# Optimization experiments

Hardware: AMD Instinct MI355X
Metric: run time of the kernel (lower is better)

## Reference

```python
import jax, jax.numpy as jnp
import numpy as np

B, T, D, V = 2, 2048, 768, 50257
REWARD_SCALE = 0.5
DIV_WEIGHT = 0.1
EPS = 1e-8  # torch cosine_similarity eps


def setup_inputs() -> dict:
    key = jax.random.key(0)
    k1, k2, k3, k4 = jax.random.split(key, 4)
    return {
        "pass2_hidden": jax.random.normal(k1, (B, T, D), dtype=jnp.float32),
        "pass3_hidden": jax.random.normal(k2, (B, T, D), dtype=jnp.float32),
        "W": jax.random.normal(k3, (V, D), dtype=jnp.float32) * 0.02,  # lm_head weight [V, D]
        "targets": jax.random.randint(k4, (B, T), 0, V, dtype=jnp.int64),
    }


def _masked_ce(hidden, W, targets):
    # hidden: [B,T,D], W: [V,D], targets: [B,T] with ignore_index=-1
    logits = jnp.einsum('btd,vd->btv', hidden, W).reshape(B * T, V)
    t = targets.reshape(B * T)
    valid = t != -1
    safe_t = jnp.where(valid, t, 0)
    logp = jax.nn.log_softmax(logits, axis=-1)
    nll = -jnp.take_along_axis(logp, safe_t[:, None], axis=-1)[:, 0]
    nll = jnp.where(valid, nll, 0.0)
    return nll.sum() / jnp.maximum(valid.sum(), 1).astype(nll.dtype)


def reference(pass2_hidden, pass3_hidden, W, targets):
    # pass 2 CE computed under no_grad in the original
    loss_p2 = jax.lax.stop_gradient(_masked_ce(pass2_hidden, W, targets))
    loss_p3 = _masked_ce(pass3_hidden, W, targets)
    reward_loss = -REWARD_SCALE * (loss_p2 - loss_p3)

    p2 = jax.lax.stop_gradient(pass2_hidden.reshape(B * T, D))  # .detach()
    p3 = pass3_hidden.reshape(B * T, D)
    n2 = jnp.maximum(jnp.linalg.norm(p2, axis=-1), EPS)
    n3 = jnp.maximum(jnp.linalg.norm(p3, axis=-1), EPS)
    cos = jnp.sum(p2 * p3, axis=-1) / (n2 * n3)
    divergence_loss = DIV_WEIGHT * cos.mean()
    return reward_loss + divergence_loss
```

## Files before the change

kernel.cpp:

```cpp
#include <hip/hip_runtime.h>
#include <math.h>

#define BT     4096
#define M_TOT  8192
#define KDIM   768
#define VDIM   50257
#define NBLK   393
#define KCH    24
#define REWARD_SCALE 0.5
#define DIV_WEIGHT   0.1
#define EPS_COS      1e-8f
#define LOG2E        1.44269504088896340736f

typedef _Float16 half8 __attribute__((ext_vector_type(8)));
typedef float    f32x4 __attribute__((ext_vector_type(4)));

#define A_FRAGS (64*KCH*8*64)
#define W_FRAGS (NBLK*KCH*8*64)

__device__ __forceinline__ void g2l16(const short* g, short* l) {
    __builtin_amdgcn_global_load_lds(
        (const __attribute__((address_space(1))) unsigned int*)(const void*)g,
        (__attribute__((address_space(3))) unsigned int*)(void*)l,
        16, 0, 0);
}

__global__ __launch_bounds__(256)
void convert_A_kernel(const float* __restrict__ p2, const float* __restrict__ p3,
                      short* __restrict__ Ahi)
{
    __shared__ float Ls[128][36];
    const int mb = blockIdx.x;
    const int k0 = blockIdx.y;
    const int tid = threadIdx.x;

#pragma unroll
    for (int p = 0; p < 4; ++p) {
        int i = p * 1024 + tid * 4;
        int r = i >> 5;
        int c = i & 31;
        int m = mb * 128 + r;
        const float* src = (m < BT) ? (p2 + (size_t)m * KDIM)
                                    : (p3 + (size_t)(m - BT) * KDIM);
        float4 v = *(const float4*)(src + k0 * 32 + c);
        *(float4*)&Ls[r][c] = v;
    }
    __syncthreads();

    size_t base = ((size_t)(mb * KCH + k0) * 8) * 64;
#pragma unroll
    for (int h = 0; h < 2; ++h) {
        int f    = tid + h * 256;
        int lane = f & 63;
        int tile = f >> 6;
        int row  = tile * 16 + (lane & 15);
        int kq   = (lane >> 4) * 8;
        half8 out;
#pragma unroll
        for (int j = 0; j < 8; ++j) out[j] = (_Float16)Ls[row][kq + j];
        *(half8*)(Ahi + (base + f) * 8) = out;
    }
}

__global__ __launch_bounds__(256)
void convert_W_kernel(const float* __restrict__ W, short* __restrict__ Whi)
{
    __shared__ float Ls[128][36];
    const int nb = blockIdx.x;
    const int k0 = blockIdx.y;
    const int tid = threadIdx.x;

#pragma unroll
    for (int p = 0; p < 4; ++p) {
        int i = p * 1024 + tid * 4;
        int r = i >> 5;
        int c = i & 31;
        int v = nb * 128 + r;
        float4 val = make_float4(0.f, 0.f, 0.f, 0.f);
        if (v < VDIM) val = *(const float4*)(W + (size_t)v * KDIM + k0 * 32 + c);
        *(float4*)&Ls[r][c] = val;
    }
    __syncthreads();

    size_t base = ((size_t)(nb * KCH + k0) * 8) * 64;
#pragma unroll
    for (int h = 0; h < 2; ++h) {
        int f    = tid + h * 256;
        int lane = f & 63;
        int tile = f >> 6;
        int row  = tile * 16 + (lane & 15);
        int kq   = (lane >> 4) * 8;
        half8 out;
#pragma unroll
        for (int j = 0; j < 8; ++j) out[j] = (_Float16)(Ls[row][kq + j] * LOG2E);
        *(half8*)(Whi + (base + f) * 8) = out;
    }
}

__global__ __launch_bounds__(256, 4)
void gemm_f16_kernel(const short* __restrict__ Ahi, const short* __restrict__ Whi,
                     double* __restrict__ g_sumexp)
{
    __shared__ __align__(16) short As[2][8][64][8];
    __shared__ float rowsum[128];

    const int tid    = threadIdx.x;
    const int lane   = tid & 63;
    const int wave   = tid >> 6;
    const int wave_m = wave >> 1;
    const int wave_n = wave & 1;
    const int mb = blockIdx.x;
    const int nb = blockIdx.y;

    if (tid < 128) rowsum[tid] = 0.0f;

    f32x4 acc[4][4];
#pragma unroll
    for (int i = 0; i < 4; ++i)
#pragma unroll
        for (int j = 0; j < 4; ++j) acc[i][j] = (f32x4)0.0f;

    const short* Ablk  = Ahi + (size_t)mb * KCH * 4096 + lane * 8;
    const short* Bbase = Whi + (size_t)nb * KCH * 4096
                             + ((size_t)(wave_n * 4) * 64 + lane) * 8;

#define STAGEA(k0_, buf_)                                                     \
    {                                                                         \
        _Pragma("unroll")                                                     \
        for (int j = 0; j < 2; ++j) {                                         \
            int c = wave * 2 + j;                                             \
            g2l16(Ablk + (size_t)((k0_) * 8 + c) * 512, &As[buf_][c][lane][0]);\
        }                                                                     \
    }

    half8 b[2][4];
    STAGEA(0, 0);
#pragma unroll
    for (int tn = 0; tn < 4; ++tn)
        b[0][tn] = *(const half8*)(Bbase + tn * 512);

#pragma unroll 2
    for (int k0 = 0; k0 < KCH; ++k0) {
        const int buf = k0 & 1;
        __syncthreads();
        if (k0 + 1 < KCH) {
            STAGEA(k0 + 1, buf ^ 1);
#pragma unroll
            for (int tn = 0; tn < 4; ++tn)
                b[buf ^ 1][tn] = *(const half8*)(Bbase + (size_t)(k0 + 1) * 4096
                                                 + tn * 512);
        }
        half8 a[4];
#pragma unroll
        for (int tm = 0; tm < 4; ++tm)
            a[tm] = *(const half8*)&As[buf][wave_m * 4 + tm][lane][0];
#pragma unroll
        for (int tm = 0; tm < 4; ++tm)
#pragma unroll
            for (int tn = 0; tn < 4; ++tn)
                acc[tm][tn] = __builtin_amdgcn_mfma_f32_16x16x32_f16(
                                  a[tm], b[buf][tn], acc[tm][tn], 0, 0, 0);
    }
#undef STAGEA

    __syncthreads();
    const int colBase = nb * 128 + wave_n * 64;
    const int quad = lane >> 4;
    const int cidx = lane & 15;
#pragma unroll
    for (int tm = 0; tm < 4; ++tm) {
#pragma unroll
        for (int r = 0; r < 4; ++r) {
            float s = 0.0f;
#pragma unroll
            for (int tn = 0; tn < 4; ++tn) {
                int col = colBase + tn * 16 + cidx;
                if (col < VDIM) s += __builtin_amdgcn_exp2f(acc[tm][tn][r]);
            }
            s += __shfl_xor(s, 1);
            s += __shfl_xor(s, 2);
            s += __shfl_xor(s, 4);
            s += __shfl_xor(s, 8);
            if (cidx == 0) {
                int row = wave_m * 64 + tm * 16 + quad * 4 + r;
                atomicAdd(&rowsum[row], s);
            }
        }
    }
    __syncthreads();
    if (tid < 128) {
        atomicAdd(&g_sumexp[(size_t)mb * 128 + tid], (double)rowsum[tid]);
    }
}

#define BM 128
#define BN 128
#define BK 16
#define LDPAD 4
__global__ __launch_bounds__(256)
void logits_expsum_kernel(const float* __restrict__ p2,
                          const float* __restrict__ p3,
                          const float* __restrict__ W,
                          double* __restrict__ g_sumexp)
{
    __shared__ float As[BK][BM + LDPAD];
    __shared__ float Bsh[BK][BN + LDPAD];
    __shared__ float rowsum[BM];

    const int tid     = threadIdx.x;
    const int rowBase = blockIdx.y * BM;
    const int colBase = blockIdx.x * BN;

    if (tid < BM) rowsum[tid] = 0.0f;

    float acc[8][8];
#pragma unroll
    for (int i = 0; i < 8; ++i)
#pragma unroll
        for (int j = 0; j < 8; ++j) acc[i][j] = 0.0f;

    const int ty = tid >> 4;
    const int tx = tid & 15;
    const int r0 = ty * 8;
    const int c0 = tx * 4;

    for (int k0 = 0; k0 < KDIM; k0 += BK) {
        __syncthreads();
#pragma unroll
        for (int l = 0; l < 2; ++l) {
            int id  = tid + l * 256;
            int row = id >> 2;
            int kq  = id & 3;
            int m   = rowBase + row;
            const float* src = (m < BT) ? (p2 + (size_t)m * KDIM)
                                        : (p3 + (size_t)(m - BT) * KDIM);
            float4 v = *(const float4*)(src + k0 + kq * 4);
            As[kq * 4 + 0][row] = v.x;
            As[kq * 4 + 1][row] = v.y;
            As[kq * 4 + 2][row] = v.z;
            As[kq * 4 + 3][row] = v.w;
        }
#pragma unroll
        for (int l = 0; l < 2; ++l) {
            int id  = tid + l * 256;
            int row = id >> 2;
            int kq  = id & 3;
            int c   = colBase + row;
            int cs  = (c < VDIM) ? c : (VDIM - 1);
            float4 v = *(const float4*)(W + (size_t)cs * KDIM + k0 + kq * 4);
            Bsh[kq * 4 + 0][row] = v.x;
            Bsh[kq * 4 + 1][row] = v.y;
            Bsh[kq * 4 + 2][row] = v.z;
            Bsh[kq * 4 + 3][row] = v.w;
        }
        __syncthreads();
#pragma unroll
        for (int kk = 0; kk < BK; ++kk) {
            float a[8], bb[8];
            *(float4*)&a[0]  = *(const float4*)&As[kk][r0];
            *(float4*)&a[4]  = *(const float4*)&As[kk][r0 + 4];
            *(float4*)&bb[0] = *(const float4*)&Bsh[kk][c0];
            *(float4*)&bb[4] = *(const float4*)&Bsh[kk][64 + c0];
#pragma unroll
            for (int i = 0; i < 8; ++i)
#pragma unroll
                for (int j = 0; j < 8; ++j)
                    acc[i][j] = fmaf(a[i], bb[j], acc[i][j]);
        }
    }

    __syncthreads();
#pragma unroll
    for (int i = 0; i < 8; ++i) {
        float s = 0.0f;
#pragma unroll
        for (int j = 0; j < 8; ++j) {
            int c = colBase + ((j < 4) ? (c0 + j) : (64 + c0 + (j - 4)));
            if (c < VDIM) s += expf(acc[i][j]);
        }
        atomicAdd(&rowsum[r0 + i], s);
    }
    __syncthreads();
    if (tid < BM) {
        atomicAdd(&g_sumexp[rowBase + tid], (double)rowsum[tid]);
    }
}

__global__ __launch_bounds__(256)
void finalize_tokens_kernel(const float* __restrict__ p2,
                            const float* __restrict__ p3,
                            const float* __restrict__ W,
                            const int*   __restrict__ targets,
                            const double* __restrict__ g_sumexp,
                            double* __restrict__ tokvals)
{
    const int t   = blockIdx.x;
    const int tid = threadIdx.x;
    const int tg  = targets[t];
    const bool valid = (tg >= 0);
    const float* w = W + (size_t)(valid ? tg : 0) * KDIM;
    const float* a = p2 + (size_t)t * KDIM;
    const float* b = p3 + (size_t)t * KDIM;

    float s22 = 0.f, s33 = 0.f, s23 = 0.f, s2w = 0.f, s3w = 0.f;
    for (int i = tid; i < KDIM; i += 256) {
        float x = a[i], y = b[i], ww = w[i];
        s22 = fmaf(x, x, s22);
        s33 = fmaf(y, y, s33);
        s23 = fmaf(x, y, s23);
        s2w = fmaf(x, ww, s2w);
        s3w = fmaf(y, ww, s3w);
    }
#pragma unroll
    for (int off = 32; off > 0; off >>= 1) {
        s22 += __shfl_down(s22, off);
        s33 += __shfl_down(s33, off);
        s23 += __shfl_down(s23, off);
        s2w += __shfl_down(s2w, off);
        s3w += __shfl_down(s3w, off);
    }
    __shared__ float sm[5][4];
    const int wv = tid >> 6, lane = tid & 63;
    if (lane == 0) {
        sm[0][wv] = s22; sm[1][wv] = s33; sm[2][wv] = s23;
        sm[3][wv] = s2w; sm[4][wv] = s3w;
    }
    __syncthreads();
    if (tid == 0) {
        float S22 = sm[0][0] + sm[0][1] + sm[0][2] + sm[0][3];
        float S33 = sm[1][0] + sm[1][1] + sm[1][2] + sm[1][3];
        float S23 = sm[2][0] + sm[2][1] + sm[2][2] + sm[2][3];
        float S2w = sm[3][0] + sm[3][1] + sm[3][2] + sm[3][3];
        float S3w = sm[4][0] + sm[4][1] + sm[4][2] + sm[4][3];

        float n2 = fmaxf(sqrtf(S22), EPS_COS);
        float n3 = fmaxf(sqrtf(S33), EPS_COS);

        double4 out;
        out.x = valid ? (log(g_sumexp[t])      - (double)S2w) : 0.0;
        out.y = valid ? (log(g_sumexp[BT + t]) - (double)S3w) : 0.0;
        out.z = (double)(S23 / (n2 * n3));
        out.w = valid ? 1.0 : 0.0;
        *(double4*)(tokvals + 4 * (size_t)t) = out;
    }
}

__global__ __launch_bounds__(1024)
void final_scalar_kernel(const double* __restrict__ tokvals,
                         float* __restrict__ out)
{
    const int tid = threadIdx.x;
    double s0 = 0.0, s1 = 0.0, s2 = 0.0, s3 = 0.0;
    for (int t = tid; t < BT; t += 1024) {
        double4 v = *(const double4*)(tokvals + 4 * (size_t)t);
        s0 += v.x; s1 += v.y; s2 += v.z; s3 += v.w;
    }
#pragma unroll
    for (int off = 32; off > 0; off >>= 1) {
        s0 += __shfl_down(s0, off);
        s1 += __shfl_down(s1, off);
        s2 += __shfl_down(s2, off);
        s3 += __shfl_down(s3, off);
    }
    __shared__ double sm[4][16];
    const int wv = tid >> 6, lane = tid & 63;
    if (lane == 0) { sm[0][wv] = s0; sm[1][wv] = s1; sm[2][wv] = s2; sm[3][wv] = s3; }
    __syncthreads();
    if (tid == 0) {
        double S0 = 0, S1 = 0, S2 = 0, S3 = 0;
#pragma unroll
        for (int i = 0; i < 16; ++i) { S0 += sm[0][i]; S1 += sm[1][i]; S2 += sm[2][i]; S3 += sm[3][i]; }
        double cnt = (S3 > 0.0) ? S3 : 1.0;
        double loss_p2 = S0 / cnt;
        double loss_p3 = S1 / cnt;
        double reward_loss = -REWARD_SCALE * (loss_p2 - loss_p3);
        double divergence  =  DIV_WEIGHT * (S2 / (double)BT);
        out[0] = (float)(reward_loss + divergence);
    }
}

extern "C" void kernel_launch(void* const* d_in, const int* in_sizes, int n_in,
                              void* d_out, int out_size, void* d_ws, size_t ws_size,
                              hipStream_t stream)
{
    const float* p2  = (const float*)d_in[0];
    const float* p3  = (const float*)d_in[1];
    const float* W   = (const float*)d_in[2];
    const int*   tgt = (const int*)d_in[3];

    double* g_sumexp = (double*)d_ws;
    double* tokvals  = g_sumexp + M_TOT;
    char*   fragbase = (char*)d_ws + 196608;

    hipMemsetAsync(d_ws, 0, 65536, stream);

    const size_t need = 196608 + (size_t)A_FRAGS * 16 + (size_t)W_FRAGS * 16;
    if (ws_size >= need) {
        short* Ahi = (short*)fragbase;
        short* Whi = Ahi + (size_t)A_FRAGS * 8;

        convert_A_kernel<<<dim3(64, KCH), dim3(256), 0, stream>>>(p2, p3, Ahi);
        convert_W_kernel<<<dim3(NBLK, KCH), dim3(256), 0, stream>>>(W, Whi);
        gemm_f16_kernel<<<dim3(64, NBLK), dim3(256), 0, stream>>>(Ahi, Whi, g_sumexp);
    } else {
        logits_expsum_kernel<<<dim3(NBLK, 64), dim3(256), 0, stream>>>(p2, p3, W, g_sumexp);
    }

    finalize_tokens_kernel<<<dim3(BT), dim3(256), 0, stream>>>(
        p2, p3, W, tgt, g_sumexp, tokvals);

    final_scalar_kernel<<<dim3(1), dim3(1024), 0, stream>>>(tokvals, (float*)d_out);
}
```

Measured before the change: 908.1 us.

## Double GEMM M-tile to 256 rows and defer log-sum-exp to final reduction

The f16 MFMA GEMM block now covers 256 rows instead of 128, so each W fragment loaded from global memory is reused across twice as many rows and half as many blocks are launched. The register accumulator doubles and the occupancy hint drops from 4 to 2 blocks per CU. The per-token finalize kernel no longer reads g_sumexp; it stores only dot products, and the log of the sum-exp is applied in the final scalar kernel, so the dot kernel can run before the GEMM. The risk is that higher register pressure and lower occupancy hurt latency hiding.

```diff
diff --git a/kernel.cpp b/kernel.cpp
--- a/kernel.cpp
+++ b/kernel.cpp
@@ -97,47 +97,49 @@
     }
 }
 
-__global__ __launch_bounds__(256, 4)
+__global__ __launch_bounds__(256, 2)
 void gemm_f16_kernel(const short* __restrict__ Ahi, const short* __restrict__ Whi,
                      double* __restrict__ g_sumexp)
 {
-    __shared__ __align__(16) short As[2][8][64][8];
-    __shared__ float rowsum[128];
+    __shared__ __align__(16) short As[2][16][64][8];
+    __shared__ float rowsum[256];
 
     const int tid    = threadIdx.x;
     const int lane   = tid & 63;
     const int wave   = tid >> 6;
     const int wave_m = wave >> 1;
     const int wave_n = wave & 1;
-    const int mb = blockIdx.x;
-    const int nb = blockIdx.y;
-
-    if (tid < 128) rowsum[tid] = 0.0f;
-
-    f32x4 acc[4][4];
-#pragma unroll
-    for (int i = 0; i < 4; ++i)
+    const int mb2 = blockIdx.x;
+    const int nb  = blockIdx.y;
+
+    rowsum[tid] = 0.0f;
+
+    f32x4 acc[8][4];
+#pragma unroll
+    for (int i = 0; i < 8; ++i)
 #pragma unroll
         for (int j = 0; j < 4; ++j) acc[i][j] = (f32x4)0.0f;
 
-    const short* Ablk  = Ahi + (size_t)mb * KCH * 4096 + lane * 8;
+    const size_t Aroot = (size_t)(2 * mb2) * KCH * 4096;
     const short* Bbase = Whi + (size_t)nb * KCH * 4096
                              + ((size_t)(wave_n * 4) * 64 + lane) * 8;
 
 #define STAGEA(k0_, buf_)                                                     \
     {                                                                         \
         _Pragma("unroll")                                                     \
-        for (int j = 0; j < 2; ++j) {                                         \
-            int c = wave * 2 + j;                                             \
-            g2l16(Ablk + (size_t)((k0_) * 8 + c) * 512, &As[buf_][c][lane][0]);\
+        for (int j = 0; j < 4; ++j) {                                         \
+            int c = wave * 4 + j;                                             \
+            const short* gsrc = Ahi + Aroot + (size_t)(c >> 3) * KCH * 4096   \
+                              + (size_t)((k0_) * 8 + (c & 7)) * 512 + lane * 8;\
+            g2l16(gsrc, &As[buf_][c][lane][0]);                               \
         }                                                                     \
     }
 
-    half8 b[2][4];
+    half8 bcur[4], bnxt[4];
     STAGEA(0, 0);
 #pragma unroll
     for (int tn = 0; tn < 4; ++tn)
-        b[0][tn] = *(const half8*)(Bbase + tn * 512);
+        bcur[tn] = *(const half8*)(Bbase + tn * 512);
 
 #pragma unroll 2
     for (int k0 = 0; k0 < KCH; ++k0) {
@@ -147,19 +149,19 @@
             STAGEA(k0 + 1, buf ^ 1);
 #pragma unroll
             for (int tn = 0; tn < 4; ++tn)
-                b[buf ^ 1][tn] = *(const half8*)(Bbase + (size_t)(k0 + 1) * 4096
-                                                 + tn * 512);
-        }
-        half8 a[4];
-#pragma unroll
-        for (int tm = 0; tm < 4; ++tm)
-            a[tm] = *(const half8*)&As[buf][wave_m * 4 + tm][lane][0];
-#pragma unroll
-        for (int tm = 0; tm < 4; ++tm)
+                bnxt[tn] = *(const half8*)(Bbase + (size_t)(k0 + 1) * 4096
+                                           + tn * 512);
+        }
+#pragma unroll
+        for (int tm = 0; tm < 8; ++tm) {
+            half8 a = *(const half8*)&As[buf][wave_m * 8 + tm][lane][0];
 #pragma unroll
             for (int tn = 0; tn < 4; ++tn)
                 acc[tm][tn] = __builtin_amdgcn_mfma_f32_16x16x32_f16(
-                                  a[tm], b[buf][tn], acc[tm][tn], 0, 0, 0);
+                                  a, bcur[tn], acc[tm][tn], 0, 0, 0);
+        }
+#pragma unroll
+        for (int tn = 0; tn < 4; ++tn) bcur[tn] = bnxt[tn];
     }
 #undef STAGEA
 
@@ -168,7 +170,7 @@
     const int quad = lane >> 4;
     const int cidx = lane & 15;
 #pragma unroll
-    for (int tm = 0; tm < 4; ++tm) {
+    for (int tm = 0; tm < 8; ++tm) {
 #pragma unroll
         for (int r = 0; r < 4; ++r) {
             float s = 0.0f;
@@ -182,15 +184,13 @@
             s += __shfl_xor(s, 4);
             s += __shfl_xor(s, 8);
             if (cidx == 0) {
-                int row = wave_m * 64 + tm * 16 + quad * 4 + r;
+                int row = wave_m * 128 + tm * 16 + quad * 4 + r;
                 atomicAdd(&rowsum[row], s);
             }
         }
     }
     __syncthreads();
-    if (tid < 128) {
-        atomicAdd(&g_sumexp[(size_t)mb * 128 + tid], (double)rowsum[tid]);
-    }
+    atomicAdd(&g_sumexp[(size_t)mb2 * 256 + tid], (double)rowsum[tid]);
 }
 
 #define BM 128
@@ -287,12 +287,11 @@
 }
 
 __global__ __launch_bounds__(256)
-void finalize_tokens_kernel(const float* __restrict__ p2,
-                            const float* __restrict__ p3,
-                            const float* __restrict__ W,
-                            const int*   __restrict__ targets,
-                            const double* __restrict__ g_sumexp,
-                            double* __restrict__ tokvals)
+void finalize_dots_kernel(const float* __restrict__ p2,
+                          const float* __restrict__ p3,
+                          const float* __restrict__ W,
+                          const int*   __restrict__ targets,
+                          double* __restrict__ tokvals)
 {
     const int t   = blockIdx.x;
     const int tid = threadIdx.x;
@@ -337,8 +336,8 @@
         float n3 = fmaxf(sqrtf(S33), EPS_COS);
 
         double4 out;
-        out.x = valid ? (log(g_sumexp[t])      - (double)S2w) : 0.0;
-        out.y = valid ? (log(g_sumexp[BT + t]) - (double)S3w) : 0.0;
+        out.x = (double)S2w;
+        out.y = (double)S3w;
         out.z = (double)(S23 / (n2 * n3));
         out.w = valid ? 1.0 : 0.0;
         *(double4*)(tokvals + 4 * (size_t)t) = out;
@@ -347,13 +346,19 @@
 
 __global__ __launch_bounds__(1024)
 void final_scalar_kernel(const double* __restrict__ tokvals,
+                         const double* __restrict__ g_sumexp,
                          float* __restrict__ out)
 {
     const int tid = threadIdx.x;
     double s0 = 0.0, s1 = 0.0, s2 = 0.0, s3 = 0.0;
     for (int t = tid; t < BT; t += 1024) {
         double4 v = *(const double4*)(tokvals + 4 * (size_t)t);
-        s0 += v.x; s1 += v.y; s2 += v.z; s3 += v.w;
+        if (v.w > 0.0) {
+            s0 += log(g_sumexp[t])      - v.x;
+            s1 += log(g_sumexp[BT + t]) - v.y;
+            s3 += 1.0;
+        }
+        s2 += v.z;
     }
 #pragma unroll
     for (int off = 32; off > 0; off >>= 1) {
@@ -401,13 +406,12 @@
 
         convert_A_kernel<<<dim3(64, KCH), dim3(256), 0, stream>>>(p2, p3, Ahi);
         convert_W_kernel<<<dim3(NBLK, KCH), dim3(256), 0, stream>>>(W, Whi);
-        gemm_f16_kernel<<<dim3(64, NBLK), dim3(256), 0, stream>>>(Ahi, Whi, g_sumexp);
+        finalize_dots_kernel<<<dim3(BT), dim3(256), 0, stream>>>(p2, p3, W, tgt, tokvals);
+        gemm_f16_kernel<<<dim3(32, NBLK), dim3(256), 0, stream>>>(Ahi, Whi, g_sumexp);
+        final_scalar_kernel<<<dim3(1), dim3(1024), 0, stream>>>(tokvals, g_sumexp, (float*)d_out);
     } else {
         logits_expsum_kernel<<<dim3(NBLK, 64), dim3(256), 0, stream>>>(p2, p3, W, g_sumexp);
-    }
-
-    finalize_tokens_kernel<<<dim3(BT), dim3(256), 0, stream>>>(
-        p2, p3, W, tgt, g_sumexp, tokvals);
-
-    final_scalar_kernel<<<dim3(1), dim3(1024), 0, stream>>>(tokvals, (float*)d_out);
-}
+        finalize_dots_kernel<<<dim3(BT), dim3(256), 0, stream>>>(p2, p3, W, tgt, tokvals);
+        final_scalar_kernel<<<dim3(1), dim3(1024), 0, stream>>>(tokvals, g_sumexp, (float*)d_out);
+    }
+}
```

Result: slower. 969.2 us (+6.7%).
